# Kernel optimization log

Measured on AMD Instinct MI355X. Metric: run time of the kernel, lower is better.

## Reference

```python
import jax, jax.numpy as jnp
import numpy as np

B, L, S, E, D = 16, 2048, 2048, 64, 64

def setup_inputs() -> dict:
    key = jax.random.key(0)
    k1, k2, k3, k4 = jax.random.split(key, 4)
    queries = jax.random.normal(k1, (B, L, E), dtype=jnp.float32)
    keys = jax.random.normal(k2, (B, S, E), dtype=jnp.float32)
    values = jax.random.normal(k3, (B, S, D), dtype=jnp.float32)
    mlp = jax.random.normal(k4, (L, L), dtype=jnp.float32)  # learned seq-mix matrix
    return {"queries": queries, "keys": keys, "values": values, "mlp": mlp}

def reference(queries, keys, values, mlp):
    # scale = 1/sqrt(E) (self.scale is None)
    E_dim = queries.shape[-1]
    scale = 1.0 / jnp.sqrt(jnp.asarray(E_dim, dtype=queries.dtype))
    # scores: [B, L, S]
    scores = jnp.einsum('ble,bse->bls', queries, keys)
    # dropout omitted (eval mode / attention_dropout=0)
    A = jax.nn.softmax(scale * scores, axis=-1)
    # attention output: [B, L, D]
    V = jnp.einsum('bls,bsd->bld', A, values)
    # learned sequence-mixing: [B, L, D] -> [B, P, D] with P == L
    out = jnp.einsum('bld,pl->bpd', V, mlp)
    return out
```

## Files before the change

kernel.cpp:

```cpp
#include <hip/hip_runtime.h>

#define NB 16
#define NL 2048
#define NS 2048
#define NE 64
#define ND 64

typedef float floatx4 __attribute__((ext_vector_type(4)));
typedef _Float16 half8 __attribute__((ext_vector_type(8)));
typedef __fp16 half2v __attribute__((ext_vector_type(2)));

union H8 { half8 v; half2v h2[4]; };

__device__ __forceinline__ half8 cvt8(floatx4 a, floatx4 b) {
  H8 h;
  h.h2[0] = __builtin_amdgcn_cvt_pkrtz(a[0], a[1]);
  h.h2[1] = __builtin_amdgcn_cvt_pkrtz(a[2], a[3]);
  h.h2[2] = __builtin_amdgcn_cvt_pkrtz(b[0], b[1]);
  h.h2[3] = __builtin_amdgcn_cvt_pkrtz(b[2], b[3]);
  return h.v;
}

__device__ __forceinline__ void async16(void* l, const void* g) {
  __builtin_amdgcn_global_load_lds((__attribute__((address_space(1))) void*)g,
                                   (__attribute__((address_space(3))) void*)l, 16, 0, 0);
}

#define B1_WAIT8  { asm volatile("s_waitcnt vmcnt(8)" ::: "memory"); __builtin_amdgcn_s_barrier(); }
#define B1_WAIT0  { asm volatile("s_waitcnt vmcnt(0)" ::: "memory"); __builtin_amdgcn_s_barrier(); }
#define B2_LGKM   { asm volatile("s_waitcnt lgkmcnt(0)" ::: "memory"); __builtin_amdgcn_s_barrier(); }

__device__ __forceinline__ int kinv(int y) {
  return (y & 0x23) | ((y & 8) << 1) | ((y & 4) << 1) | ((y & 16) >> 2);
}

__global__ __launch_bounds__(256) void prep_k(const float* __restrict__ V,
                                              const float* __restrict__ K,
                                              _Float16* __restrict__ Vt,
                                              _Float16* __restrict__ Kh,
                                              int do_k) {
  __shared__ __align__(16) _Float16 Vl[64][72];
  const int bid = blockIdx.x;
  const int t = threadIdx.x;

  if (bid < 512) {
    const int b = bid >> 5;
    const int s0 = (bid & 31) * 64;
    {
      int sl = t & 63;
      int dg = t >> 6;
      const float* src = V + ((size_t)(b * NS + s0 + sl)) * ND + dg * 16;
      int x = kinv(sl);
      #pragma unroll
      for (int c = 0; c < 4; ++c) {
        floatx4 v = *(const floatx4*)(src + c * 4);
        #pragma unroll
        for (int e = 0; e < 4; ++e) Vl[dg * 16 + c * 4 + e][x] = (_Float16)v[e];
      }
    }
    __syncthreads();
    {
      int d = t & 63;
      int xg = t >> 6;
      int dk = (d & 7) << 3;
      #pragma unroll
      for (int h = 0; h < 2; ++h) {
        int x = xg * 16 + h * 8;
        half8 v = *(const half8*)&Vl[d][x];
        *(half8*)(Vt + ((size_t)(b * ND + d)) * NS + s0 + (x ^ dk)) = v;
      }
    }
  } else {
    if (!do_k) return;
    int c = (bid - 512) * 256 + t;
    int j = c & 7;
    int s = (c >> 3) & (NS - 1);
    int b = c >> 14;
    const float* src = K + ((size_t)(b * NS + s)) * NE + j * 8;
    half8 h = cvt8(*(const floatx4*)src, *(const floatx4*)(src + 4));
    *(half8*)(Kh + ((size_t)(b * NS + s)) * NE + (j ^ (s & 7)) * 8) = h;
  }
}

template<bool KH16>
__global__ __launch_bounds__(256) void attn_k(const float* __restrict__ Q,
                                              const void* __restrict__ Ksrc,
                                              const _Float16* __restrict__ Vtp,
                                              _Float16* __restrict__ Vatt,
                                              const float* __restrict__ Mf,
                                              _Float16* __restrict__ Mh) {
  __shared__ __align__(16) char smem[65536];
  const int tid = threadIdx.x;
  const int wid = tid >> 6, lane = tid & 63;
  const int lr = lane & 15, lg = lane >> 4;
  const int g = wid & 1;
  const int qh = wid >> 1;
  const int b = blockIdx.y;
  const int qbase = blockIdx.x * 64 + qh * 32;
  const _Float16* Kh = (const _Float16*)Ksrc;
  const float* Kf = (const float*)Ksrc;

  constexpr float SC = 0.18033688f;
  half8 qf[2][2];
  #pragma unroll
  for (int sub = 0; sub < 2; ++sub)
    #pragma unroll
    for (int kk = 0; kk < 2; ++kk) {
      const float* qp = Q + ((size_t)(b * NL + qbase + sub * 16 + lr)) * NE + kk * 32 + lg * 8;
      floatx4 a = *(const floatx4*)qp, c = *(const floatx4*)(qp + 4);
      qf[sub][kk] = cvt8(a * SC, c * SC);
    }

  floatx4 oacc[2][4];
  #pragma unroll
  for (int s = 0; s < 2; ++s)
    #pragma unroll
    for (int m = 0; m < 4; ++m) oacc[s][m] = (floatx4){0.f, 0.f, 0.f, 0.f};
  float lrun[2] = {0.f, 0.f};

  auto stageV = [&](int buf, int s0) {
    #pragma unroll
    for (int i = 0; i < 4; ++i) {
      int co = (wid * 4 + i) * 1024;
      int o = co + lane * 16;
      int row = o >> 8, c16 = (o >> 4) & 15;
      async16(smem + 32768 + buf * 16384 + co,
              Vtp + ((size_t)(b * ND + row)) * NS + s0 + c16 * 8);
    }
  };
  auto stageK = [&](int buf, int s0) {
    if constexpr (KH16) {
      #pragma unroll
      for (int i = 0; i < 4; ++i) {
        int co = (wid * 4 + i) * 1024;
        int o = co + lane * 16;
        int row = o >> 7, c8 = (o >> 4) & 7;
        async16(smem + buf * 16384 + co,
                Kh + ((size_t)(b * NS + s0 + row)) * NE + c8 * 8);
      }
    } else {
      int row = tid >> 1, cg = (tid & 1) * 32;
      const float* kp = Kf + ((size_t)(b * NS + s0 + row)) * NE + cg;
      #pragma unroll
      for (int c = 0; c < 4; ++c) {
        half8 h = cvt8(*(const floatx4*)(kp + c * 8), *(const floatx4*)(kp + c * 8 + 4));
        int col = cg + c * 8;
        *(half8*)(smem + buf * 16384 + ((row * 128 + col * 2) ^ ((row & 7) << 4))) = h;
      }
    }
  };

  stageK(0, 0); stageV(0, 0);
  if constexpr (!KH16) __syncthreads();

  for (int t = 0; t < NS / 128; ++t) {
    int buf = t & 1;
    if (t + 1 < NS / 128) {
      stageK(buf ^ 1, (t + 1) * 128); stageV(buf ^ 1, (t + 1) * 128);
      if constexpr (KH16) B1_WAIT8 else __syncthreads();
    } else {
      if constexpr (KH16) B1_WAIT0
    }

    const char* kb = smem + buf * 16384;
    const char* vb = smem + 32768 + buf * 16384;

    half8 kf[4][2];
    #pragma unroll
    for (int mt = 0; mt < 4; ++mt)
      #pragma unroll
      for (int kk = 0; kk < 2; ++kk) {
        int row = g * 64 + mt * 16 + lr, col = kk * 32 + lg * 8;
        kf[mt][kk] = *(const half8*)(kb + ((row * 128 + col * 2) ^ ((row & 7) << 4)));
      }

    H8 bf[2][2];
    #pragma unroll
    for (int sub = 0; sub < 2; ++sub) {
      floatx4 sacc[4];
      #pragma unroll
      for (int mt = 0; mt < 4; ++mt) sacc[mt] = (floatx4){0.f, 0.f, 0.f, 0.f};
      __builtin_amdgcn_s_setprio(1);
      #pragma unroll
      for (int kk = 0; kk < 2; ++kk)
        #pragma unroll
        for (int mt = 0; mt < 4; ++mt)
          sacc[mt] = __builtin_amdgcn_mfma_f32_16x16x32_f16(kf[mt][kk], qf[sub][kk], sacc[mt], 0, 0, 0);
      __builtin_amdgcn_s_setprio(0);

      float lloc = 0.f;
      half2v w[4][2];
      #pragma unroll
      for (int mt = 0; mt < 4; ++mt) {
        float p0 = __builtin_amdgcn_exp2f(sacc[mt][0]);
        float p1 = __builtin_amdgcn_exp2f(sacc[mt][1]);
        float p2 = __builtin_amdgcn_exp2f(sacc[mt][2]);
        float p3 = __builtin_amdgcn_exp2f(sacc[mt][3]);
        lloc += (p0 + p1) + (p2 + p3);
        w[mt][0] = __builtin_amdgcn_cvt_pkrtz(p0, p1);
        w[mt][1] = __builtin_amdgcn_cvt_pkrtz(p2, p3);
      }
      lloc += __shfl_xor(lloc, 16, 64);
      lloc += __shfl_xor(lloc, 32, 64);
      lrun[sub] += lloc;
      #pragma unroll
      for (int kk = 0; kk < 2; ++kk) {
        bf[sub][kk].h2[0] = w[2 * kk][0];
        bf[sub][kk].h2[1] = w[2 * kk][1];
        bf[sub][kk].h2[2] = w[2 * kk + 1][0];
        bf[sub][kk].h2[3] = w[2 * kk + 1][1];
      }
    }

    __builtin_amdgcn_s_setprio(1);
    #pragma unroll
    for (int kk = 0; kk < 2; ++kk)
      #pragma unroll
      for (int mt = 0; mt < 4; ++mt) {
        int row = mt * 16 + lr;
        int off = ((kk * 32 + lg * 8) * 2) ^ ((row & 7) << 4);
        half8 vt = *(const half8*)(vb + row * 256 + g * 128 + off);
        oacc[0][mt] = __builtin_amdgcn_mfma_f32_16x16x32_f16(vt, bf[0][kk].v, oacc[0][mt], 0, 0, 0);
        oacc[1][mt] = __builtin_amdgcn_mfma_f32_16x16x32_f16(vt, bf[1][kk].v, oacc[1][mt], 0, 0, 0);
      }
    __builtin_amdgcn_s_setprio(0);
    if constexpr (KH16) B2_LGKM else __syncthreads();
  }

  {
    char* red = smem + qh * 16384;
    if (g == 1) {
      #pragma unroll
      for (int sub = 0; sub < 2; ++sub)
        #pragma unroll
        for (int mt = 0; mt < 4; ++mt)
          *(floatx4*)(red + lane * 144 + (sub * 4 + mt) * 16) = oacc[sub][mt];
      if (lg == 0) {
        *(float*)(red + 9216 + lr * 8) = lrun[0];
        *(float*)(red + 9216 + lr * 8 + 4) = lrun[1];
      }
    }
    __syncthreads();
    if (g == 0) {
      #pragma unroll
      for (int sub = 0; sub < 2; ++sub) {
        float lt = lrun[sub] + *(const float*)(red + 9216 + lr * 8 + sub * 4);
        float inv = __builtin_amdgcn_rcpf(lt);
        int l = qbase + sub * 16 + lr;
        #pragma unroll
        for (int mt = 0; mt < 4; ++mt) {
          floatx4 o = oacc[sub][mt] + *(const floatx4*)(red + lane * 144 + (sub * 4 + mt) * 16);
          #pragma unroll
          for (int r = 0; r < 4; ++r) {
            int d = mt * 16 + lg * 4 + r;
            int lsw = (l & ~63) | ((l & 63) ^ ((d & 7) << 3));
            Vatt[((size_t)(b * ND + d)) * NL + lsw] = (_Float16)(o[r] * inv);
          }
        }
      }
    }
  }

  if constexpr (KH16) {
    int mb = blockIdx.y * 32 + blockIdx.x;
    #pragma unroll
    for (int q = 0; q < 4; ++q) {
      int c = mb * 1024 + q * 256 + tid;
      int j = c & 255, p = c >> 8;
      const float* src = Mf + (size_t)p * NL + j * 8;
      half8 h = cvt8(*(const floatx4*)src, *(const floatx4*)(src + 4));
      int jo = (j & ~7) | ((j & 7) ^ (p & 7));
      *(half8*)(Mh + (size_t)p * NL + jo * 8) = h;
    }
  }
}

template<bool A16>
__global__ __launch_bounds__(256) void mix_k(const void* __restrict__ Asrc,
                                             const _Float16* __restrict__ Bsrc,
                                             float* __restrict__ out) {
  __shared__ __align__(16) char smem[65536];
  const int tid = threadIdx.x;
  const int wid = tid >> 6, lane = tid & 63;
  const int lr = lane & 15, lg = lane >> 4;
  const int kh = wid & 1;
  const int mw = wid >> 1;
  const int p0 = blockIdx.x * 64;
  const int b = blockIdx.y;
  const _Float16* Ah = (const _Float16*)Asrc;
  const float* Af = (const float*)Asrc;

  floatx4 acc[2][4];
  #pragma unroll
  for (int mt = 0; mt < 2; ++mt)
    #pragma unroll
    for (int nt = 0; nt < 4; ++nt) acc[mt][nt] = (floatx4){0.f, 0.f, 0.f, 0.f};

  auto stage = [&](int buf, int t) {
    int k0 = kh * (NL / 2) + t * 64;
    if constexpr (A16) {
      #pragma unroll
      for (int i = 0; i < 4; ++i) {
        int co = (mw * 4 + i) * 1024;
        int o = co + lane * 16;
        int row = o >> 7, c8 = (o >> 4) & 7;
        async16(smem + kh * 16384 + buf * 8192 + co,
                Ah + ((size_t)(p0 + row)) * NL + k0 + c8 * 8);
      }
    } else {
      int row = (lane & 31) + mw * 32, cg = (lane >> 5) * 32;
      const float* ap = Af + ((size_t)(p0 + row)) * NL + k0 + cg;
      #pragma unroll
      for (int c = 0; c < 4; ++c) {
        half8 h = cvt8(*(const floatx4*)(ap + c * 8), *(const floatx4*)(ap + c * 8 + 4));
        int col = cg + c * 8;
        *(half8*)(smem + kh * 16384 + buf * 8192 +
                  ((row * 128 + col * 2) ^ ((row & 7) << 4))) = h;
      }
    }
    #pragma unroll
    for (int i = 0; i < 4; ++i) {
      int co = (mw * 4 + i) * 1024;
      int o = co + lane * 16;
      int row = o >> 7, c8 = (o >> 4) & 7;
      async16(smem + 32768 + kh * 16384 + buf * 8192 + co,
              Bsrc + ((size_t)(b * ND + row)) * NL + k0 + c8 * 8);
    }
  };

  stage(0, 0);
  if constexpr (!A16) __syncthreads();

  for (int t = 0; t < 16; ++t) {
    int buf = t & 1;
    if (t + 1 < 16) {
      stage(buf ^ 1, t + 1);
      if constexpr (A16) B1_WAIT8 else __syncthreads();
    } else {
      if constexpr (A16) B1_WAIT0
    }
    const char* ab = smem + kh * 16384 + buf * 8192;
    const char* bb = smem + 32768 + kh * 16384 + buf * 8192;
    #pragma unroll
    for (int kk = 0; kk < 2; ++kk) {
      int col = kk * 32 + lg * 8;
      half8 af[2];
      #pragma unroll
      for (int mt = 0; mt < 2; ++mt) {
        int row = mw * 32 + mt * 16 + lr;
        af[mt] = *(const half8*)(ab + ((row * 128 + col * 2) ^ ((row & 7) << 4)));
      }
      __builtin_amdgcn_s_setprio(1);
      #pragma unroll
      for (int nt = 0; nt < 4; ++nt) {
        int row = nt * 16 + lr;
        half8 bfr = *(const half8*)(bb + ((row * 128 + col * 2) ^ ((row & 7) << 4)));
        #pragma unroll
        for (int mt = 0; mt < 2; ++mt)
          acc[mt][nt] = __builtin_amdgcn_mfma_f32_16x16x32_f16(af[mt], bfr, acc[mt][nt], 0, 0, 0);
      }
      __builtin_amdgcn_s_setprio(0);
    }
    if constexpr (A16) B2_LGKM else __syncthreads();
  }

  if (kh == 1) {
    #pragma unroll
    for (int mt = 0; mt < 2; ++mt)
      #pragma unroll
      for (int nt = 0; nt < 4; ++nt) {
        int idx = mt * 4 + nt;
        *(floatx4*)(smem + mw * 8192 + lane * 128 + ((idx ^ (lane & 7)) * 16)) = acc[mt][nt];
      }
  }
  __syncthreads();
  if (kh == 0) {
    #pragma unroll
    for (int mt = 0; mt < 2; ++mt)
      #pragma unroll
      for (int nt = 0; nt < 4; ++nt) {
        int idx = mt * 4 + nt;
        acc[mt][nt] += *(const floatx4*)(smem + mw * 8192 + lane * 128 + ((idx ^ (lane & 7)) * 16));
        #pragma unroll
        for (int r = 0; r < 4; ++r) {
          int p = p0 + mw * 32 + mt * 16 + lg * 4 + r;
          int d = nt * 16 + lr;
          out[((size_t)(b * NL + p)) * ND + d] = acc[mt][nt][r];
        }
      }
  }
}

extern "C" void kernel_launch(void* const* d_in, const int* in_sizes, int n_in,
                              void* d_out, int out_size, void* d_ws, size_t ws_size,
                              hipStream_t stream) {
  (void)in_sizes; (void)n_in; (void)out_size;
  const float* Q = (const float*)d_in[0];
  const float* K = (const float*)d_in[1];
  const float* V = (const float*)d_in[2];
  const float* M = (const float*)d_in[3];
  float* out = (float*)d_out;

  char* ws = (char*)d_ws;
  _Float16* Vtp  = (_Float16*)ws;
  _Float16* Vatt = (_Float16*)(ws + (4u << 20));
  _Float16* Kh   = (_Float16*)(ws + (8u << 20));
  _Float16* Mh   = (_Float16*)(ws + (12u << 20));
  bool big = ws_size >= (size_t)(20u << 20);

  if (big) {
    prep_k<<<1536, 256, 0, stream>>>(V, K, Vtp, Kh, 1);
    attn_k<true><<<dim3(32, 16), 256, 0, stream>>>(Q, Kh, Vtp, Vatt, M, Mh);
    mix_k<true><<<dim3(32, 16), 256, 0, stream>>>(Mh, Vatt, out);
  } else {
    prep_k<<<512, 256, 0, stream>>>(V, K, Vtp, Kh, 0);
    attn_k<false><<<dim3(32, 16), 256, 0, stream>>>(Q, K, Vtp, Vatt, nullptr, nullptr);
    mix_k<false><<<dim3(32, 16), 256, 0, stream>>>(M, Vatt, out);
  }
}
```

Baseline: 56.59 us.

## Split KV tile four ways per wave, MFMA row sums, remap block-to-XCD mapping

Each of the four waves now owns all 64 queries of the block and a 32-key slice of every 128-key tile, where before the block used two query halves times two key halves. This reuses each V fragment across four query subtiles and removes the per-tile shuffle reduction of softmax row sums, which is now computed with an MFMA against a ones vector. Precomputed LDS offsets replace per-iteration address math. Block indices in both kernels are remapped so that blocks sharing a batch or an M tile land near each other, likely to improve cache locality across XCDs. In exchange, register use rises with 16 output accumulators per wave, and the final cross-wave reduction writes three partial buffers to LDS.

Result: no change. 56.60 us (+0.0%).

```diff
diff --git a/kernel.cpp b/kernel.cpp
--- a/kernel.cpp
+++ b/kernel.cpp
@@ -93,17 +93,18 @@
   const int tid = threadIdx.x;
   const int wid = tid >> 6, lane = tid & 63;
   const int lr = lane & 15, lg = lane >> 4;
-  const int g = wid & 1;
-  const int qh = wid >> 1;
-  const int b = blockIdx.y;
-  const int qbase = blockIdx.x * 64 + qh * 32;
+  const int g = wid;
+  const int L = blockIdx.y * 32 + blockIdx.x;
+  const int b = (L & 7) * 2 + ((L >> 3) & 1);
+  const int qx = L >> 4;
+  const int qbase = qx * 64;
   const _Float16* Kh = (const _Float16*)Ksrc;
   const float* Kf = (const float*)Ksrc;
 
   constexpr float SC = 0.18033688f;
-  half8 qf[2][2];
-  #pragma unroll
-  for (int sub = 0; sub < 2; ++sub)
+  half8 qf[4][2];
+  #pragma unroll
+  for (int sub = 0; sub < 4; ++sub)
     #pragma unroll
     for (int kk = 0; kk < 2; ++kk) {
       const float* qp = Q + ((size_t)(b * NL + qbase + sub * 16 + lr)) * NE + kk * 32 + lg * 8;
@@ -111,12 +112,31 @@
       qf[sub][kk] = cvt8(a * SC, c * SC);
     }
 
-  floatx4 oacc[2][4];
-  #pragma unroll
-  for (int s = 0; s < 2; ++s)
+  half8 ones;
+  #pragma unroll
+  for (int i = 0; i < 8; ++i) ones[i] = (_Float16)1.0f;
+
+  floatx4 oacc[4][4], lacc[4];
+  #pragma unroll
+  for (int s = 0; s < 4; ++s) {
+    lacc[s] = (floatx4){0.f, 0.f, 0.f, 0.f};
     #pragma unroll
     for (int m = 0; m < 4; ++m) oacc[s][m] = (floatx4){0.f, 0.f, 0.f, 0.f};
-  float lrun[2] = {0.f, 0.f};
+  }
+
+  int kOff[2][2], vOff[4];
+  #pragma unroll
+  for (int mt = 0; mt < 2; ++mt)
+    #pragma unroll
+    for (int kk = 0; kk < 2; ++kk) {
+      int row = g * 32 + mt * 16 + lr, col = kk * 32 + lg * 8;
+      kOff[mt][kk] = (row * 128 + col * 2) ^ ((row & 7) << 4);
+    }
+  #pragma unroll
+  for (int mt = 0; mt < 4; ++mt) {
+    int row = mt * 16 + lr;
+    vOff[mt] = row * 256 + (g >> 1) * 128 + (((g & 1) * 64 + lg * 16) ^ ((row & 7) << 4));
+  }
 
   auto stageV = [&](int buf, int s0) {
     #pragma unroll
@@ -165,91 +185,90 @@
     const char* kb = smem + buf * 16384;
     const char* vb = smem + 32768 + buf * 16384;
 
-    half8 kf[4][2];
-    #pragma unroll
-    for (int mt = 0; mt < 4; ++mt)
-      #pragma unroll
-      for (int kk = 0; kk < 2; ++kk) {
-        int row = g * 64 + mt * 16 + lr, col = kk * 32 + lg * 8;
-        kf[mt][kk] = *(const half8*)(kb + ((row * 128 + col * 2) ^ ((row & 7) << 4)));
-      }
-
-    H8 bf[2][2];
-    #pragma unroll
-    for (int sub = 0; sub < 2; ++sub) {
-      floatx4 sacc[4];
-      #pragma unroll
-      for (int mt = 0; mt < 4; ++mt) sacc[mt] = (floatx4){0.f, 0.f, 0.f, 0.f};
+    half8 kf[2][2];
+    #pragma unroll
+    for (int mt = 0; mt < 2; ++mt)
+      #pragma unroll
+      for (int kk = 0; kk < 2; ++kk)
+        kf[mt][kk] = *(const half8*)(kb + kOff[mt][kk]);
+
+    H8 bf[4];
+    #pragma unroll
+    for (int sub = 0; sub < 4; ++sub) {
+      floatx4 sacc[2];
+      #pragma unroll
+      for (int mt = 0; mt < 2; ++mt) sacc[mt] = (floatx4){0.f, 0.f, 0.f, 0.f};
       __builtin_amdgcn_s_setprio(1);
       #pragma unroll
       for (int kk = 0; kk < 2; ++kk)
         #pragma unroll
-        for (int mt = 0; mt < 4; ++mt)
+        for (int mt = 0; mt < 2; ++mt)
           sacc[mt] = __builtin_amdgcn_mfma_f32_16x16x32_f16(kf[mt][kk], qf[sub][kk], sacc[mt], 0, 0, 0);
       __builtin_amdgcn_s_setprio(0);
 
-      float lloc = 0.f;
-      half2v w[4][2];
-      #pragma unroll
-      for (int mt = 0; mt < 4; ++mt) {
-        float p0 = __builtin_amdgcn_exp2f(sacc[mt][0]);
-        float p1 = __builtin_amdgcn_exp2f(sacc[mt][1]);
-        float p2 = __builtin_amdgcn_exp2f(sacc[mt][2]);
-        float p3 = __builtin_amdgcn_exp2f(sacc[mt][3]);
-        lloc += (p0 + p1) + (p2 + p3);
-        w[mt][0] = __builtin_amdgcn_cvt_pkrtz(p0, p1);
-        w[mt][1] = __builtin_amdgcn_cvt_pkrtz(p2, p3);
-      }
-      lloc += __shfl_xor(lloc, 16, 64);
-      lloc += __shfl_xor(lloc, 32, 64);
-      lrun[sub] += lloc;
-      #pragma unroll
-      for (int kk = 0; kk < 2; ++kk) {
-        bf[sub][kk].h2[0] = w[2 * kk][0];
-        bf[sub][kk].h2[1] = w[2 * kk][1];
-        bf[sub][kk].h2[2] = w[2 * kk + 1][0];
-        bf[sub][kk].h2[3] = w[2 * kk + 1][1];
-      }
+      float p00 = __builtin_amdgcn_exp2f(sacc[0][0]);
+      float p01 = __builtin_amdgcn_exp2f(sacc[0][1]);
+      float p02 = __builtin_amdgcn_exp2f(sacc[0][2]);
+      float p03 = __builtin_amdgcn_exp2f(sacc[0][3]);
+      float p10 = __builtin_amdgcn_exp2f(sacc[1][0]);
+      float p11 = __builtin_amdgcn_exp2f(sacc[1][1]);
+      float p12 = __builtin_amdgcn_exp2f(sacc[1][2]);
+      float p13 = __builtin_amdgcn_exp2f(sacc[1][3]);
+      bf[sub].h2[0] = __builtin_amdgcn_cvt_pkrtz(p00, p01);
+      bf[sub].h2[1] = __builtin_amdgcn_cvt_pkrtz(p02, p03);
+      bf[sub].h2[2] = __builtin_amdgcn_cvt_pkrtz(p10, p11);
+      bf[sub].h2[3] = __builtin_amdgcn_cvt_pkrtz(p12, p13);
     }
 
     __builtin_amdgcn_s_setprio(1);
     #pragma unroll
-    for (int kk = 0; kk < 2; ++kk)
-      #pragma unroll
-      for (int mt = 0; mt < 4; ++mt) {
-        int row = mt * 16 + lr;
-        int off = ((kk * 32 + lg * 8) * 2) ^ ((row & 7) << 4);
-        half8 vt = *(const half8*)(vb + row * 256 + g * 128 + off);
-        oacc[0][mt] = __builtin_amdgcn_mfma_f32_16x16x32_f16(vt, bf[0][kk].v, oacc[0][mt], 0, 0, 0);
-        oacc[1][mt] = __builtin_amdgcn_mfma_f32_16x16x32_f16(vt, bf[1][kk].v, oacc[1][mt], 0, 0, 0);
-      }
+    for (int mt = 0; mt < 4; ++mt) {
+      half8 vt = *(const half8*)(vb + vOff[mt]);
+      #pragma unroll
+      for (int sub = 0; sub < 4; ++sub)
+        oacc[sub][mt] = __builtin_amdgcn_mfma_f32_16x16x32_f16(vt, bf[sub].v, oacc[sub][mt], 0, 0, 0);
+    }
+    #pragma unroll
+    for (int sub = 0; sub < 4; ++sub)
+      lacc[sub] = __builtin_amdgcn_mfma_f32_16x16x32_f16(ones, bf[sub].v, lacc[sub], 0, 0, 0);
     __builtin_amdgcn_s_setprio(0);
+
     if constexpr (KH16) B2_LGKM else __syncthreads();
   }
 
   {
-    char* red = smem + qh * 16384;
-    if (g == 1) {
-      #pragma unroll
-      for (int sub = 0; sub < 2; ++sub)
-        #pragma unroll
-        for (int mt = 0; mt < 4; ++mt)
-          *(floatx4*)(red + lane * 144 + (sub * 4 + mt) * 16) = oacc[sub][mt];
+    char* red = smem;
+    if (g != 0) {
+      #pragma unroll
+      for (int sub = 0; sub < 4; ++sub)
+        #pragma unroll
+        for (int mt = 0; mt < 4; ++mt) {
+          int idx = sub * 4 + mt;
+          *(floatx4*)(red + (g - 1) * 16384 + lane * 256 + ((idx ^ (lane & 15)) * 16)) = oacc[sub][mt];
+        }
       if (lg == 0) {
-        *(float*)(red + 9216 + lr * 8) = lrun[0];
-        *(float*)(red + 9216 + lr * 8 + 4) = lrun[1];
+        #pragma unroll
+        for (int sub = 0; sub < 4; ++sub)
+          *(float*)(red + 49152 + (g - 1) * 256 + lr * 16 + sub * 4) = lacc[sub][0];
       }
     }
     __syncthreads();
     if (g == 0) {
       #pragma unroll
-      for (int sub = 0; sub < 2; ++sub) {
-        float lt = lrun[sub] + *(const float*)(red + 9216 + lr * 8 + sub * 4);
+      for (int sub = 0; sub < 4; ++sub) {
+        float lt = lacc[sub][0];
+        #pragma unroll
+        for (int gg = 0; gg < 3; ++gg)
+          lt += *(const float*)(red + 49152 + gg * 256 + lr * 16 + sub * 4);
         float inv = __builtin_amdgcn_rcpf(lt);
         int l = qbase + sub * 16 + lr;
         #pragma unroll
         for (int mt = 0; mt < 4; ++mt) {
-          floatx4 o = oacc[sub][mt] + *(const floatx4*)(red + lane * 144 + (sub * 4 + mt) * 16);
+          floatx4 o = oacc[sub][mt];
+          int idx = sub * 4 + mt;
+          #pragma unroll
+          for (int gg = 0; gg < 3; ++gg)
+            o += *(const floatx4*)(red + gg * 16384 + lane * 256 + ((idx ^ (lane & 15)) * 16));
           #pragma unroll
           for (int r = 0; r < 4; ++r) {
             int d = mt * 16 + lg * 4 + r;
@@ -285,8 +304,10 @@
   const int lr = lane & 15, lg = lane >> 4;
   const int kh = wid & 1;
   const int mw = wid >> 1;
-  const int p0 = blockIdx.x * 64;
-  const int b = blockIdx.y;
+  const int L = blockIdx.y * 32 + blockIdx.x;
+  const int i = L >> 3;
+  const int p0 = ((L & 7) * 4 + (i & 3)) * 64;
+  const int b = i >> 2;
   const _Float16* Ah = (const _Float16*)Asrc;
   const float* Af = (const float*)Asrc;
 
@@ -300,8 +321,8 @@
     int k0 = kh * (NL / 2) + t * 64;
     if constexpr (A16) {
       #pragma unroll
-      for (int i = 0; i < 4; ++i) {
-        int co = (mw * 4 + i) * 1024;
+      for (int i2 = 0; i2 < 4; ++i2) {
+        int co = (mw * 4 + i2) * 1024;
         int o = co + lane * 16;
         int row = o >> 7, c8 = (o >> 4) & 7;
         async16(smem + kh * 16384 + buf * 8192 + co,
@@ -319,8 +340,8 @@
       }
     }
     #pragma unroll
-    for (int i = 0; i < 4; ++i) {
-      int co = (mw * 4 + i) * 1024;
+    for (int i2 = 0; i2 < 4; ++i2) {
+      int co = (mw * 4 + i2) * 1024;
       int o = co + lane * 16;
       int row = o >> 7, c8 = (o >> 4) & 7;
       async16(smem + 32768 + kh * 16384 + buf * 8192 + co,
```
